# Optimization experiments

Measured on AMD Instinct MI355X. Metric: run time of the kernel, lower is better.

The kernel has to match this reference:

```python
import jax, jax.numpy as jnp
import numpy as np

B, J, DIMS, T = 1024, 22, 3, 100
C = J * DIMS            # 66 channels
H, HD = 8, 64           # heads, head_dim
E = H * HD              # 512
LOCAL_WINDOW = 5
EPS = 1e-5


def setup_inputs() -> dict:
    key = jax.random.key(0)
    ks = jax.random.split(key, 32)
    s = 0.02  # small init scale for learned params

    # kinematic-chain skeleton adjacency mask (buffer, symmetric 0/1)
    am = np.zeros((J, J), dtype=np.float32)
    for i in range(J - 1):
        am[i, i + 1] = 1.0
        am[i + 1, i] = 1.0
    adj_mask = jnp.asarray(am)

    # banded temporal mask: tril(+w) * triu(-w)
    tm = np.tril(np.ones((T, T), np.float32), LOCAL_WINDOW) * np.triu(np.ones((T, T), np.float32), -LOCAL_WINDOW)
    traj_mask = jnp.asarray(tm)

    def lin(k, din, dout):
        k1, k2 = jax.random.split(k)
        return (jax.random.normal(k1, (din, dout), jnp.float32) * s,
                jax.random.normal(k2, (dout,), jnp.float32) * s)

    # spatial->temporal attention: query_dim=C (66), key_dim=T (100)
    st_wq, st_bq = lin(ks[1], C, E)
    st_wk, st_bk = lin(ks[2], T, E)
    st_wv, st_bv = lin(ks[3], T, E)
    st_wo, st_bo = lin(ks[4], E, C)
    # temporal->spatial attention: query_dim=T (100), key_dim=C (66)
    ts_wq, ts_bq = lin(ks[5], T, E)
    ts_wk, ts_bk = lin(ks[6], C, E)
    ts_wv, ts_bv = lin(ks[7], C, E)
    ts_wo, ts_bo = lin(ks[8], E, T)

    return {
        "x": jax.random.normal(ks[0], (B, C, T), jnp.float32),
        "adj_mask": adj_mask,
        "s_adj": jnp.eye(J, dtype=jnp.float32),  # torch init: eye
        "traj_mask": traj_mask,
        # torch init is zeros; use small random so the temporal branch is non-degenerate
        "t_adj": jax.random.normal(ks[9], (T, T), jnp.float32) * s,
        "st_wq": st_wq, "st_bq": st_bq, "st_wk": st_wk, "st_bk": st_bk,
        "st_wv": st_wv, "st_bv": st_bv, "st_wo": st_wo, "st_bo": st_bo,
        "ts_wq": ts_wq, "ts_bq": ts_bq, "ts_wk": ts_wk, "ts_bk": ts_bk,
        "ts_wv": ts_wv, "ts_bv": ts_bv, "ts_wo": ts_wo, "ts_bo": ts_bo,
        "ln_alpha": jnp.ones((1, C, 1), jnp.float32),
        "ln_beta": jnp.zeros((1, C, 1), jnp.float32),
        "fc_w": jax.random.normal(ks[10], (T, T), jnp.float32) * s,  # torch Linear weight [out,in]
        "fc_b": jax.random.normal(ks[11], (T,), jnp.float32) * s,
    }


def _cross_attn(q, kv, wq, bq, wk, bk, wv, bv, wo, bo):
    # q: [B, Lq, qdim], kv: [B, Lk, kdim] -> [B, Lq, qdim]
    b = q.shape[0]
    Q = (q @ wq + bq).reshape(b, -1, H, HD)
    K = (kv @ wk + bk).reshape(b, -1, H, HD)
    V = (kv @ wv + bv).reshape(b, -1, H, HD)
    scores = jnp.einsum('bqhd,bkhd->bhqk', Q, K) / jnp.sqrt(jnp.float32(HD))
    attn = jax.nn.softmax(scores, axis=-1)
    out = jnp.einsum('bhqk,bkhd->bqhd', attn, V).reshape(b, -1, E)
    return out @ wo + bo


def reference(x, adj_mask, s_adj, traj_mask, t_adj,
              st_wq, st_bq, st_wk, st_bk, st_wv, st_bv, st_wo, st_bo,
              ts_wq, ts_bq, ts_wk, ts_bk, ts_wv, ts_bv, ts_wo, ts_bo,
              ln_alpha, ln_beta, fc_w, fc_b):
    b, c, t = x.shape
    j = c // DIMS

    # --- SpatialGC: symmetric degree-normalized masked adjacency conv ---
    deg = adj_mask.sum(axis=1)
    dis = jnp.where(deg > 0, deg ** -0.5, 0.0)
    A = s_adj * (adj_mask * dis[:, None] * dis[None, :])        # [J,J]
    spatial = jnp.einsum('vj,bjct->bvct', A, x.reshape(b, j, DIMS, t)).reshape(b, c, t)

    # --- TemporalGC: banded learned temporal adjacency ---
    temporal = jnp.einsum('ft,bnt->bnf', t_adj * traj_mask, x)   # [B,C,T]

    # --- CrossAttentiveGC ---
    sp_seq = spatial.transpose(0, 2, 1)                          # [B,T,C] spatial tokens
    tp_seq = temporal                                            # [B,C,T] temporal tokens
    enh_sp = _cross_attn(sp_seq, tp_seq, st_wq, st_bq, st_wk, st_bk, st_wv, st_bv, st_wo, st_bo)  # [B,T,C]
    enh_tp = _cross_attn(tp_seq, sp_seq, ts_wq, ts_bq, ts_wk, ts_bk, ts_wv, ts_bv, ts_wo, ts_bo)  # [B,C,T]
    combined = (enh_sp.reshape(b, t, j, DIMS).transpose(0, 2, 3, 1)
                + enh_tp.reshape(b, j, DIMS, t)).reshape(b, c, t)

    # --- LN over channel dim (dim=1) with biased variance ---
    mean = combined.mean(axis=1, keepdims=True)
    var = ((combined - mean) ** 2).mean(axis=1, keepdims=True)
    y = (combined - mean) / jnp.sqrt(var + EPS)
    y = y * ln_alpha + ln_beta

    # --- residual + Linear over the seq dim, tanh ---
    out = jnp.einsum('bct,ft->bcf', y + x, fc_w) + fc_b
    return jnp.tanh(out)
```

## Files before the change

### kernel.cpp

```cpp
#include <hip/hip_runtime.h>
#include <hip/hip_bf16.h>
#include <math.h>
#include <stdint.h>

typedef __hip_bfloat16 bf16;
typedef __attribute__((ext_vector_type(8))) short short8;
typedef __attribute__((ext_vector_type(4))) short short4v;
typedef __attribute__((ext_vector_type(4))) float f32x4;
typedef __attribute__((ext_vector_type(4))) unsigned int uint4v;
union PF { uint4v u; short8 s; };

#define CC 66
#define TT 100
#define JJ 22
#define HH 8
#define HD 64
#define EE 512
#define CPAD 101

#define SPT_R 112
#define SPT_S 96
#define TP_R 80
#define TP_S 128

#define W_STWK 0
#define W_STWQ 65536
#define W_TSWK 114688
#define W_TSWQ 163840
#define W_VST  229376
#define W_VTS  311296
#define W_TOTAL 397312

#define TOKSP 0
#define TOKTP 11648
#define G0Z1  22528
#define G0Z2  27648
#define G0Z3  34816
#define G1Z1  45056
#define G1Z2  52224
#define G1Z3  57344
#define SMEM_SH 71680

__device__ __forceinline__ bf16 f2b(float v){ return __float2bfloat16(v); }
__device__ __forceinline__ short sb(float v){ __hip_bfloat16 h = __float2bfloat16(v); return *(short*)&h; }
__device__ __forceinline__ unsigned int pk2(float a, float b){
  unsigned short ua = (unsigned short)sb(a), ub = (unsigned short)sb(b);
  return (unsigned int)ua | ((unsigned int)ub << 16);
}

__device__ __forceinline__ void tr_body(
    const float* __restrict__ src, bf16* __restrict__ dst,
    int Rsrc, int Csrc, int JP, int IP, int blk, int tid)
{
  int o = blk*256 + tid;
  if (o >= JP*IP) return;
  int j = o / IP, i = o - j*IP;
  float v = (j < Csrc && i < Rsrc) ? src[(long)i*Csrc + j] : 0.f;
  dst[o] = f2b(v);
}

__device__ __forceinline__ void wt_body(
    const float* __restrict__ wv, const float* __restrict__ wo,
    bf16* __restrict__ dst, int OUT, int KDIM, int OP, int KP, int blk, int tid)
{
  int idx = blk*256 + tid;
  if (idx >= 8*OP*KP) return;
  int o = idx % OP;
  int hk = idx / OP;
  int k = hk % KP, h = hk / KP;
  float acc = 0.f;
  if (o < OUT && k < KDIM) {
    const float* wvp = wv + (long)k*EE + h*64;
    const float* wop = wo + (long)(h*64)*OUT + o;
    #pragma unroll 8
    for (int d = 0; d < 64; ++d) acc += wvp[d] * wop[(long)d*OUT];
  }
  dst[(long)h*OP*KP + (long)o*KP + k] = f2b(acc);
}

__global__ __launch_bounds__(256) void k_wprep(
    const float* __restrict__ st_wk, const float* __restrict__ st_wq,
    const float* __restrict__ ts_wk, const float* __restrict__ ts_wq,
    const float* __restrict__ st_wv, const float* __restrict__ st_wo,
    const float* __restrict__ ts_wv, const float* __restrict__ ts_wo,
    const float* __restrict__ st_bo, const float* __restrict__ st_bv,
    const float* __restrict__ ts_bo, const float* __restrict__ ts_bv,
    bf16* __restrict__ wsec, float* __restrict__ bias2)
{
  const int blk = blockIdx.x, tid = threadIdx.x;
  if      (blk <  256) tr_body(st_wk, wsec + W_STWK, TT, EE, EE, 128, blk,      tid);
  else if (blk <  448) tr_body(st_wq, wsec + W_STWQ, CC, EE, EE,  96, blk-256,  tid);
  else if (blk <  640) tr_body(ts_wk, wsec + W_TSWK, CC, EE, EE,  96, blk-448,  tid);
  else if (blk <  896) tr_body(ts_wq, wsec + W_TSWQ, TT, EE, EE, 128, blk-640,  tid);
  else if (blk < 1216) wt_body(st_wv, st_wo, wsec + W_VST, CC, TT,  80, 128, blk-896,  tid);
  else if (blk < 1552) wt_body(ts_wv, ts_wo, wsec + W_VTS, TT, CC, 112,  96, blk-1216, tid);
  else {
    if (tid < 128) {
      int c = tid; float a = 0.f;
      if (c < CC) {
        a = st_bo[c];
        for (int e = 0; e < EE; ++e) a += st_bv[e] * st_wo[(long)e*CC + c];
      }
      bias2[tid] = a;
    } else {
      int t = tid - 128; float a = 0.f;
      if (t < TT) {
        a = ts_bo[t];
        for (int e = 0; e < EE; ++e) a += ts_bv[e] * ts_wo[(long)e*TT + t];
      }
      bias2[tid] = a;
    }
  }
}

__global__ __launch_bounds__(256) void k_prep(
    const float* __restrict__ x, const float* __restrict__ adj,
    const float* __restrict__ sadj, const float* __restrict__ tmask,
    const float* __restrict__ tadj,
    bf16* __restrict__ spT_all, bf16* __restrict__ tp_all)
{
  __shared__ float s_x[CC*TT];
  __shared__ float s_Mt[TT*TT];
  __shared__ float s_A[JJ*JJ];
  __shared__ float s_dis[JJ];
  const int b = blockIdx.x, tid = threadIdx.x;
  const long bb = (long)b * (CC*TT);

  if (tid < JJ) {
    float dsum = 0.f;
    for (int i = 0; i < JJ; ++i) dsum += adj[tid*JJ + i];
    s_dis[tid] = dsum > 0.f ? rsqrtf(dsum) : 0.f;
  }
  for (int o = tid; o < CC*TT; o += 256) s_x[o] = x[bb + o];
  for (int o = tid; o < TT*TT; o += 256) {
    int f = o / TT, t = o - f*TT;
    s_Mt[t*TT + f] = tadj[o] * tmask[o];
  }
  __syncthreads();
  for (int o = tid; o < JJ*JJ; o += 256) {
    int v = o / JJ, j = o - v*JJ;
    s_A[o] = sadj[o] * adj[o] * s_dis[v] * s_dis[j];
  }
  __syncthreads();

  bf16* spT = spT_all + (long)b * (SPT_R*SPT_S);
  bf16* tp  = tp_all  + (long)b * (TP_R*TP_S);

  for (int o = tid; o < 28*SPT_S; o += 256) {
    int t4 = o / SPT_S, c = o - t4*SPT_S;
    int t = t4*4;
    float ax=0.f, ay=0.f, az=0.f, aw=0.f;
    if (t < TT && c < CC) {
      int v = c/3, dd = c - v*3;
      for (int j = 0; j < JJ; ++j) {
        float av = s_A[v*JJ + j];
        float4 xv = *(const float4*)(s_x + (j*3+dd)*TT + t);
        ax += av*xv.x; ay += av*xv.y; az += av*xv.z; aw += av*xv.w;
      }
    }
    spT[(t  )*SPT_S + c] = f2b(ax);
    spT[(t+1)*SPT_S + c] = f2b(ay);
    spT[(t+2)*SPT_S + c] = f2b(az);
    spT[(t+3)*SPT_S + c] = f2b(aw);
  }
  for (int o = tid; o < TP_R*32; o += 256) {
    int n = o >> 5, f4 = o & 31;
    int f = f4*4;
    float ax=0.f, ay=0.f, az=0.f, aw=0.f;
    if (n < CC && f < TT) {
      for (int t = 0; t < TT; ++t) {
        float xv = s_x[n*TT + t];
        float4 w = *(const float4*)(s_Mt + t*TT + f);
        ax += xv*w.x; ay += xv*w.y; az += xv*w.z; aw += xv*w.w;
      }
    }
    short4v pk;
    pk.x = sb(ax); pk.y = sb(ay); pk.z = sb(az); pk.w = sb(aw);
    *(short4v*)(tp + n*TP_S + f) = pk;
  }
}

template<int Nt, int KCH, int SA, int SB>
__device__ __forceinline__ void build_kq(
    const short* __restrict__ W, const short* __restrict__ Tok,
    short* __restrict__ Z, const float* __restrict__ rowbias,
    int gw, int ln, int qd)
{
  const int mi = gw & 3;
  const int d0 = mi*16 + qd*4;
  const short* ap = W + (long)(mi*16 + ln)*SA;
  short8 af[KCH];
  #pragma unroll
  for (int kc = 0; kc < KCH; ++kc) af[kc] = *(const short8*)(ap + qd*8 + kc*32);
  float rb0=0.f, rb1=0.f, rb2=0.f, rb3=0.f;
  if (rowbias) { rb0=rowbias[d0]; rb1=rowbias[d0+1]; rb2=rowbias[d0+2]; rb3=rowbias[d0+3]; }
  constexpr int NU = (Nt + 1) / 2;
  #pragma unroll
  for (int u = 0; u < NU; ++u) {
    const int ni = (gw >> 2) + 2*u;
    if (ni < Nt) {
      const int row = ni*16 + ln;
      const short* bp = Tok + (long)row*SB;
      f32x4 acc = {0.f,0.f,0.f,0.f};
      #pragma unroll
      for (int kc = 0; kc < KCH; ++kc)
        acc = __builtin_amdgcn_mfma_f32_16x16x32_bf16(
            af[kc], *(const short8*)(bp + qd*8 + kc*32), acc, 0,0,0);
      short4v pk;
      pk.x = sb(acc[0]+rb0); pk.y = sb(acc[1]+rb1);
      pk.z = sb(acc[2]+rb2); pk.w = sb(acc[3]+rb3);
      *(short4v*)(Z + row*64 + (d0 ^ ((ln & 7) << 3))) = pk;
    }
  }
}

template<int Mt, int Nt, int KCH, int SA, int SB, int SZ>
__device__ __forceinline__ void build_vt(
    const short* __restrict__ Tok, const short* __restrict__ Wv,
    short* __restrict__ Z, int gw, int ln, int qd)
{
  if (gw >= Mt) return;
  const int mi = gw;
  const int k0 = mi*16 + qd*4;
  const short* ap = Tok + (long)(mi*16 + ln)*SA;
  short8 af[KCH];
  #pragma unroll
  for (int kc = 0; kc < KCH; ++kc) af[kc] = *(const short8*)(ap + qd*8 + kc*32);
  #pragma unroll
  for (int ni = 0; ni < Nt; ++ni) {
    const int row = ni*16 + ln;
    const short* bp = Wv + (long)row*SB;
    f32x4 acc = {0.f,0.f,0.f,0.f};
    #pragma unroll
    for (int kc = 0; kc < KCH; ++kc)
      acc = __builtin_amdgcn_mfma_f32_16x16x32_bf16(
          af[kc], *(const short8*)(bp + qd*8 + kc*32), acc, 0,0,0);
    short4v pk;
    pk.x = sb(acc[0]); pk.y = sb(acc[1]); pk.z = sb(acc[2]); pk.w = sb(acc[3]);
    *(short4v*)(Z + row*SZ + (k0 ^ ((ln & 7) << 3))) = pk;
  }
}

template<int A>
__device__ __forceinline__ void build_head(
    short* __restrict__ SMEM, const short* __restrict__ wsec,
    const float* __restrict__ bq, int h, int gw, int ln, int qd)
{
  constexpr int MQ  = A ? 5 : 7;
  constexpr int MKV = A ? 7 : 5;
  constexpr int MO  = A ? 7 : 5;
  constexpr int QCH = A ? 4 : 3;
  constexpr int KCH = A ? 3 : 4;
  constexpr int SWQ = A ? 128 : 96;
  constexpr int SWK = A ? 96 : 128;
  constexpr int SWV = A ? 96 : 128;
  constexpr int STQ = A ? 136 : 104;
  constexpr int STK = A ? 104 : 136;
  const short* tokq = SMEM + (A ? TOKTP : TOKSP);
  const short* tokk = SMEM + (A ? TOKSP : TOKTP);
  short* Z1 = SMEM + (A ? G1Z1 : G0Z1);
  short* Z2 = SMEM + (A ? G1Z2 : G0Z2);
  short* Z3 = SMEM + (A ? G1Z3 : G0Z3);
  const short* wkT = wsec + (A ? W_TSWK : W_STWK);
  const short* wqT = wsec + (A ? W_TSWQ : W_STWQ);
  const short* wvt = wsec + (A ? W_VTS  : W_VST);
  const int base = h * HD;
  build_kq<MKV, KCH, SWK, STK>(wkT + (long)base*SWK, tokk, Z1, nullptr, gw, ln, qd);
  build_kq<MQ,  QCH, SWQ, STQ>(wqT + (long)base*SWQ, tokq, Z2, bq + base, gw, ln, qd);
  build_vt<MKV, MO, KCH, STK, SWV, 128>(tokk, wvt + (long)h*(MO*16*SWV), Z3, gw, ln, qd);
}

template<int A>
__device__ __forceinline__ void chain_head(
    const short* __restrict__ SMEM, f32x4* __restrict__ accO,
    int gw, int ln, int qd)
{
  constexpr int KVR = A ? 100 : 66;
  constexpr int MQ  = A ? 5 : 7;
  constexpr int MKV = A ? 7 : 5;
  constexpr int MO  = A ? 7 : 5;
  constexpr int PCH = A ? 4 : 3;
  if (gw >= MQ) return;
  const short* Z1 = SMEM + (A ? G1Z1 : G0Z1);
  const short* Z2 = SMEM + (A ? G1Z2 : G0Z2);
  const short* Z3 = SMEM + (A ? G1Z3 : G0Z3);
  const int msk = (ln & 7) << 3;

  const short* bqp = Z2 + (gw*16 + ln)*64;
  const short8 qf0 = *(const short8*)(bqp + ((qd*8     ) ^ msk));
  const short8 qf1 = *(const short8*)(bqp + ((qd*8 + 32) ^ msk));
  f32x4 s[MKV];
  #pragma unroll
  for (int ni = 0; ni < MKV; ++ni) {
    const short* ap = Z1 + (ni*16 + ln)*64;
    f32x4 acc = {0.f,0.f,0.f,0.f};
    acc = __builtin_amdgcn_mfma_f32_16x16x32_bf16(
        *(const short8*)(ap + ((qd*8     ) ^ msk)), qf0, acc, 0,0,0);
    acc = __builtin_amdgcn_mfma_f32_16x16x32_bf16(
        *(const short8*)(ap + ((qd*8 + 32) ^ msk)), qf1, acc, 0,0,0);
    s[ni] = acc;
  }
  #pragma unroll
  for (int ni = 0; ni < MKV; ++ni) {
    #pragma unroll
    for (int r = 0; r < 4; ++r) {
      const int kv = ni*16 + qd*4 + r;
      s[ni][r] = (kv < KVR) ? s[ni][r]*0.125f : -1e30f;
    }
  }
  float mx = -1e30f;
  #pragma unroll
  for (int ni = 0; ni < MKV; ++ni)
    #pragma unroll
    for (int r = 0; r < 4; ++r) mx = fmaxf(mx, s[ni][r]);
  mx = fmaxf(mx, __shfl_xor(mx, 16));
  mx = fmaxf(mx, __shfl_xor(mx, 32));
  float l = 0.f;
  #pragma unroll
  for (int ni = 0; ni < MKV; ++ni)
    #pragma unroll
    for (int r = 0; r < 4; ++r) {
      float p = __expf(s[ni][r] - mx);
      s[ni][r] = p; l += p;
    }
  l += __shfl_xor(l, 16);
  l += __shfl_xor(l, 32);
  const float rs = 1.f / l;
  unsigned int plo[2*PCH], phi[2*PCH];
  #pragma unroll
  for (int ni = 0; ni < 2*PCH; ++ni) {
    if (ni < MKV) {
      plo[ni] = pk2(s[ni][0]*rs, s[ni][1]*rs);
      phi[ni] = pk2(s[ni][2]*rs, s[ni][3]*rs);
    } else { plo[ni] = 0u; phi[ni] = 0u; }
  }
  #pragma unroll
  for (int kc = 0; kc < PCH; ++kc) {
    PF pf;
    #pragma unroll
    for (int w = 0; w < 4; ++w) {
      const int srcLane = ln + 16*((qd & 1)*2 + (w >> 1));
      int va, vb;
      if (w & 1) {
        va = __shfl((int)phi[2*kc  ], srcLane, 64);
        vb = __shfl((int)phi[2*kc+1], srcLane, 64);
      } else {
        va = __shfl((int)plo[2*kc  ], srcLane, 64);
        vb = __shfl((int)plo[2*kc+1], srcLane, 64);
      }
      pf.u[w] = (qd < 2) ? (unsigned int)va : (unsigned int)vb;
    }
    #pragma unroll
    for (int oi = 0; oi < MO; ++oi) {
      const short* ap = Z3 + (oi*16 + ln)*128;
      short8 af = *(const short8*)(ap + ((qd*8 + kc*32) ^ msk));
      accO[oi] = __builtin_amdgcn_mfma_f32_16x16x32_bf16(af, pf.s, accO[oi], 0,0,0);
    }
  }
}

__global__ __launch_bounds__(1024, 1) void k_attn2(
    const bf16* __restrict__ spT_all, const bf16* __restrict__ tp_all,
    const bf16* __restrict__ wsec_,
    const float* __restrict__ st_bq, const float* __restrict__ ts_bq,
    const float* __restrict__ bias2, const float* __restrict__ x,
    const float* __restrict__ alpha, const float* __restrict__ beta,
    const float* __restrict__ fcw, const float* __restrict__ fcb,
    float* __restrict__ out)
{
  __shared__ __align__(16) short SMEM[SMEM_SH];
  const int b = blockIdx.x, tid = threadIdx.x;
  const long bb = (long)b * (CC*TT);
  const int wave = tid >> 6, lane = tid & 63, ln = lane & 15, qd = lane >> 4;
  const int g = wave >> 3, gw = wave & 7;
  const short* wsec = (const short*)wsec_;

  {
    const short* gsp = (const short*)(spT_all + (long)b*SPT_R*SPT_S);
    const short* gtp = (const short*)(tp_all  + (long)b*TP_R*TP_S);
    for (int o = tid; o < 112*12; o += 1024) {
      int r = o / 12, c8 = o - r*12;
      *(short8*)(SMEM + TOKSP + r*104 + c8*8) = *(const short8*)(gsp + r*SPT_S + c8*8);
    }
    for (int o = tid; o < 80*16; o += 1024) {
      int r = o >> 4, c8 = o & 15;
      *(short8*)(SMEM + TOKTP + r*136 + c8*8) = *(const short8*)(gtp + r*TP_S + c8*8);
    }
  }
  for (int o = tid; o < 80*16; o += 1024) {
    int r = o >> 4, kv = 80 + (o & 15);
    SMEM[G0Z3 + r*128 + (kv ^ ((r & 7) << 3))] = 0;
  }
  for (int o = tid; o < 112*16; o += 1024) {
    int r = o >> 4, kv = 112 + (o & 15);
    SMEM[G1Z3 + r*128 + (kv ^ ((r & 7) << 3))] = 0;
  }

  f32x4 accO[7];
  { f32x4 z = {0.f,0.f,0.f,0.f};
    #pragma unroll
    for (int i = 0; i < 7; ++i) accO[i] = z; }

  for (int h = 0; h < HH; ++h) {
    __syncthreads();
    if (g == 0) build_head<0>(SMEM, wsec, st_bq, h, gw, ln, qd);
    else        build_head<1>(SMEM, wsec, ts_bq, h, gw, ln, qd);
    __syncthreads();
    if (g == 0) chain_head<0>(SMEM, accO, gw, ln, qd);
    else        chain_head<1>(SMEM, accO, gw, ln, qd);
  }

  float* comb = (float*)(SMEM + G0Z1);
  float* s_w  = comb + 6668;
  __syncthreads();
  if (g == 0) {
    if (gw < 7) {
      const int t = gw*16 + ln;
      if (t < TT) {
        #pragma unroll
        for (int oi = 0; oi < 5; ++oi)
          #pragma unroll
          for (int r = 0; r < 4; ++r) {
            const int c = oi*16 + qd*4 + r;
            if (c < CC) comb[c*CPAD + t] = accO[oi][r];
          }
      }
    }
  } else {
    for (int o = tid - 512; o < TT*TT; o += 512) {
      int f = o / TT, t = o - f*TT;
      s_w[t*TT + f] = fcw[o];
    }
  }
  __syncthreads();
  if (g == 1 && gw < 5) {
    const int c = gw*16 + ln;
    if (c < CC) {
      #pragma unroll
      for (int oi = 0; oi < 7; ++oi)
        #pragma unroll
        for (int r = 0; r < 4; ++r) {
          const int t = oi*16 + qd*4 + r;
          if (t < TT) comb[c*CPAD + t] += accO[oi][r];
        }
    }
  }
  __syncthreads();
  for (int o = tid; o < CC*TT; o += 1024) {
    int c = o / TT, t = o - c*TT;
    comb[c*CPAD + t] += bias2[c] + bias2[128 + t];
  }
  __syncthreads();
  if (tid < 2*TT) {
    const int t = tid >> 1, hf = tid & 1;
    float part = 0.f;
    for (int c = hf; c < CC; c += 2) part += comb[c*CPAD + t];
    float mean = (part + __shfl_xor(part, 1)) * (1.f/CC);
    float vp = 0.f;
    for (int c = hf; c < CC; c += 2) { float dv = comb[c*CPAD + t] - mean; vp += dv*dv; }
    float var = (vp + __shfl_xor(vp, 1)) * (1.f/CC);
    float rstd = 1.f / sqrtf(var + 1e-5f);
    for (int c = hf; c < CC; c += 2) {
      float y = (comb[c*CPAD + t] - mean) * rstd * alpha[c] + beta[c];
      comb[c*CPAD + t] = y + x[bb + c*TT + t];
    }
  }
  __syncthreads();
  for (int o = tid; o < CC*25; o += 1024) {
    int c = o / 25, f4 = o - c*25;
    int f = f4*4;
    const float* cr = comb + c*CPAD;
    float ax=0.f, ay=0.f, az=0.f, aw=0.f;
    for (int t = 0; t < TT; ++t) {
      float xv = cr[t];
      float4 w = *(const float4*)(s_w + t*TT + f);
      ax += xv*w.x; ay += xv*w.y; az += xv*w.z; aw += xv*w.w;
    }
    float4 r4;
    r4.x = tanhf(ax + fcb[f  ]); r4.y = tanhf(ay + fcb[f+1]);
    r4.z = tanhf(az + fcb[f+2]); r4.w = tanhf(aw + fcb[f+3]);
    *(float4*)(out + bb + c*TT + f) = r4;
  }
}

__global__ __launch_bounds__(128) void k_fused(
    const float* __restrict__ x, const float* __restrict__ adj,
    const float* __restrict__ sadj, const float* __restrict__ tmask,
    const float* __restrict__ tadj,
    const float* __restrict__ st_wq, const float* __restrict__ st_bq,
    const float* __restrict__ st_wk, const float* __restrict__ st_bk,
    const float* __restrict__ st_wv, const float* __restrict__ st_bv,
    const float* __restrict__ st_wo, const float* __restrict__ st_bo,
    const float* __restrict__ ts_wq, const float* __restrict__ ts_bq,
    const float* __restrict__ ts_wk, const float* __restrict__ ts_bk,
    const float* __restrict__ ts_wv, const float* __restrict__ ts_bv,
    const float* __restrict__ ts_wo, const float* __restrict__ ts_bo,
    const float* __restrict__ alpha, const float* __restrict__ beta,
    const float* __restrict__ fcw, const float* __restrict__ fcb,
    float* __restrict__ out)
{
  __shared__ float s_sp[CC*TT];
  __shared__ float s_tp[CC*TT];
  __shared__ __align__(16) float s_kv[2*TT*HD];
  __shared__ float s_comb[CC*CPAD];
  __shared__ float s_A[JJ*JJ];
  __shared__ float s_dis[JJ];

  const int b = blockIdx.x, tid = threadIdx.x;
  const long bb = (long)b * (CC*TT);
  float* s_xs = s_comb;
  float* s_Mt = s_kv;

  if (tid < JJ) {
    float dsum = 0.f;
    for (int i = 0; i < JJ; ++i) dsum += adj[tid*JJ + i];
    s_dis[tid] = dsum > 0.f ? rsqrtf(dsum) : 0.f;
  }
  for (int o = tid; o < CC*TT; o += 128) s_xs[o] = x[bb + o];
  for (int o = tid; o < TT*TT; o += 128) {
    int f = o / TT, t = o - f*TT;
    s_Mt[t*TT + f] = tadj[o] * tmask[o];
  }
  __syncthreads();
  for (int o = tid; o < JJ*JJ; o += 128) {
    int v = o / JJ, j = o - v*JJ;
    s_A[o] = sadj[o] * adj[o] * s_dis[v] * s_dis[j];
  }
  __syncthreads();

  for (int o = tid; o < CC*TT; o += 128) {
    int c = o / TT, t = o - c*TT, v = c / 3, dd = c - v*3;
    float acc = 0.f;
    for (int j = 0; j < JJ; ++j) acc += s_A[v*JJ + j] * s_xs[(j*3 + dd)*TT + t];
    s_sp[o] = acc;
  }
  for (int o = tid; o < CC*TT; o += 128) {
    int n = o / TT, f = o - n*TT;
    float a0 = 0.f, a1 = 0.f;
    for (int t = 0; t < TT; t += 2) {
      a0 += s_xs[n*TT + t    ] * s_Mt[(t    )*TT + f];
      a1 += s_xs[n*TT + t + 1] * s_Mt[(t + 1)*TT + f];
    }
    s_tp[o] = a0 + a1;
  }
  __syncthreads();

  for (int o = tid; o < CC*TT; o += 128) {
    int c = o / TT, t = o - c*TT;
    s_comb[c*CPAD + t] = st_bo[c] + ts_bo[t];
  }

  {
    float* s_k = s_kv;
    float* s_v = s_kv + TT*HD;
    for (int h = 0; h < HH; ++h) {
      const int base = h*HD;
      __syncthreads();
      {
        const int d = tid & 63, krow = tid >> 6;
// ... 122 lines not shown
          for (int i = 0; i < 16; ++i) {
            float4 vv4 = vr4[i];
            ov[4*i  ] = ov[4*i  ]*corr + p*vv4.x;
            ov[4*i+1] = ov[4*i+1]*corr + p*vv4.y;
            ov[4*i+2] = ov[4*i+2]*corr + p*vv4.z;
            ov[4*i+3] = ov[4*i+3]*corr + p*vv4.w;
          }
          m = mn;
        }
        float rl = 1.f/l;
        #pragma unroll
        for (int d = 0; d < HD; ++d) ov[d] *= rl;
        for (int t = 0; t < TT; ++t) {
          const float* wr = ts_wo + (long)base*TT + t;
          float a0=0.f,a1=0.f,a2=0.f,a3=0.f;
          #pragma unroll
          for (int d = 0; d < HD; d += 4) {
            a0 += ov[d  ]*wr[(long)(d  )*TT]; a1 += ov[d+1]*wr[(long)(d+1)*TT];
            a2 += ov[d+2]*wr[(long)(d+2)*TT]; a3 += ov[d+3]*wr[(long)(d+3)*TT];
          }
          s_comb[q*CPAD + t] += a0+a1+a2+a3;
        }
      }
    }
  }
  __syncthreads();

  if (tid < TT) {
    const int t = tid;
    float mean = 0.f;
    for (int c = 0; c < CC; ++c) mean += s_comb[c*CPAD + t];
    mean *= (1.f/CC);
    float var = 0.f;
    for (int c = 0; c < CC; ++c) { float dv = s_comb[c*CPAD + t] - mean; var += dv*dv; }
    var *= (1.f/CC);
    float rstd = 1.f / sqrtf(var + 1e-5f);
    for (int c = 0; c < CC; ++c) {
      float y = (s_comb[c*CPAD + t] - mean) * rstd * alpha[c] + beta[c];
      s_comb[c*CPAD + t] = y + x[bb + c*TT + t];
    }
  }
  __syncthreads();

  float* s_w = s_kv;
  for (int o = tid; o < TT*TT; o += 128) {
    int f = o / TT, t = o - f*TT;
    s_w[t*TT + f] = fcw[o];
  }
  __syncthreads();

  for (int o = tid; o < CC*TT; o += 128) {
    int c = o / TT, f = o - c*TT;
    const float* cr = s_comb + c*CPAD;
    float a0 = 0.f, a1 = 0.f;
    for (int t = 0; t < TT; t += 2) {
      a0 += cr[t    ] * s_w[(t    )*TT + f];
      a1 += cr[t + 1] * s_w[(t + 1)*TT + f];
    }
    out[bb + o] = tanhf(a0 + a1 + fcb[f]);
  }
}

extern "C" void kernel_launch(void* const* d_in, const int* in_sizes, int n_in,
                              void* d_out, int out_size, void* d_ws, size_t ws_size,
                              hipStream_t stream) {
  const float* x     = (const float*)d_in[0];
  const float* adj   = (const float*)d_in[1];
  const float* sadj  = (const float*)d_in[2];
  const float* tmask = (const float*)d_in[3];
  const float* tadj  = (const float*)d_in[4];
  const float* st_wq = (const float*)d_in[5];  const float* st_bq = (const float*)d_in[6];
  const float* st_wk = (const float*)d_in[7];  const float* st_bk = (const float*)d_in[8];
  const float* st_wv = (const float*)d_in[9];  const float* st_bv = (const float*)d_in[10];
  const float* st_wo = (const float*)d_in[11]; const float* st_bo = (const float*)d_in[12];
  const float* ts_wq = (const float*)d_in[13]; const float* ts_bq = (const float*)d_in[14];
  const float* ts_wk = (const float*)d_in[15]; const float* ts_bk = (const float*)d_in[16];
  const float* ts_wv = (const float*)d_in[17]; const float* ts_bv = (const float*)d_in[18];
  const float* ts_wo = (const float*)d_in[19]; const float* ts_bo = (const float*)d_in[20];
  const float* alpha = (const float*)d_in[21]; const float* beta  = (const float*)d_in[22];
  const float* fcw   = (const float*)d_in[23]; const float* fcb   = (const float*)d_in[24];
  float* out = (float*)d_out;

  const int B = in_sizes[0] / (CC*TT);
  const size_t w_bytes   = (size_t)W_TOTAL * 2 + 1024;
  const size_t spt_bytes = (size_t)B * SPT_R * SPT_S * 2;
  const size_t tp_bytes  = (size_t)B * TP_R * TP_S * 2;
  const size_t need = w_bytes + spt_bytes + tp_bytes;

  if (ws_size >= need) {
    bf16*  wsec    = (bf16*)d_ws;
    float* bias2   = (float*)((char*)d_ws + (size_t)W_TOTAL*2);
    bf16*  spT_all = (bf16*)((char*)d_ws + w_bytes);
    bf16*  tp_all  = spT_all + (size_t)B * SPT_R * SPT_S;

    k_wprep<<<1553, 256, 0, stream>>>(st_wk, st_wq, ts_wk, ts_wq,
                                      st_wv, st_wo, ts_wv, ts_wo,
                                      st_bo, st_bv, ts_bo, ts_bv,
                                      wsec, bias2);
    k_prep<<<B, 256, 0, stream>>>(x, adj, sadj, tmask, tadj, spT_all, tp_all);
    k_attn2<<<B, 1024, 0, stream>>>(spT_all, tp_all, wsec, st_bq, ts_bq,
                                    bias2, x, alpha, beta, fcw, fcb, out);
  } else {
    k_fused<<<B, 128, 0, stream>>>(x, adj, sadj, tmask, tadj,
                                   st_wq, st_bq, st_wk, st_bk, st_wv, st_bv, st_wo, st_bo,
                                   ts_wq, ts_bq, ts_wk, ts_bk, ts_wv, ts_bv, ts_wo, ts_bo,
                                   alpha, beta, fcw, fcb, out);
  }
}
```

Measured before the change: 674.9 us.

## Run both attention directions sequentially across all 16 waves with shared-memory P matrix

Stops splitting the 16 waves into two groups that each handle one attention direction at once. Now all waves process one direction at a time, across all heads. The softmax probabilities are written to a shared-memory P buffer instead of being shuffled across lanes. The P·V output is computed as independent tiles spread over all waves and accumulated straight into the shared comb buffer, rather than kept in per-wave register accumulators. This cuts register pressure and balances work across waves, at the cost of an extra barrier per head and read-modify-write traffic on the shared comb buffer.

Measured after the change: 786.9 us. 1.17x slower.

```diff
diff --git a/kernel.cpp b/kernel.cpp
--- a/kernel.cpp
+++ b/kernel.cpp
@@ -7,8 +7,6 @@
 typedef __attribute__((ext_vector_type(8))) short short8;
 typedef __attribute__((ext_vector_type(4))) short short4v;
 typedef __attribute__((ext_vector_type(4))) float f32x4;
-typedef __attribute__((ext_vector_type(4))) unsigned int uint4v;
-union PF { uint4v u; short8 s; };
 
 #define CC 66
 #define TT 100
@@ -33,20 +31,13 @@
 
 #define TOKSP 0
 #define TOKTP 11648
-#define G0Z1  22528
-#define G0Z2  27648
-#define G0Z3  34816
-#define G1Z1  45056
-#define G1Z2  52224
-#define G1Z3  57344
-#define SMEM_SH 71680
+#define ZONES 22528
+#define PBUF  49152
+#define COMBO 64384
+#define SMEM_SH 77728
 
 __device__ __forceinline__ bf16 f2b(float v){ return __float2bfloat16(v); }
 __device__ __forceinline__ short sb(float v){ __hip_bfloat16 h = __float2bfloat16(v); return *(short*)&h; }
-__device__ __forceinline__ unsigned int pk2(float a, float b){
-  unsigned short ua = (unsigned short)sb(a), ub = (unsigned short)sb(b);
-  return (unsigned int)ua | ((unsigned int)ub << 16);
-}
 
 __device__ __forceinline__ void tr_body(
     const float* __restrict__ src, bf16* __restrict__ dst,
@@ -181,12 +172,12 @@
 }
 
 template<int Nt, int KCH, int SA, int SB>
-__device__ __forceinline__ void build_kq(
+__device__ __forceinline__ void build_kq16(
     const short* __restrict__ W, const short* __restrict__ Tok,
     short* __restrict__ Z, const float* __restrict__ rowbias,
-    int gw, int ln, int qd)
-{
-  const int mi = gw & 3;
+    int w, int ln, int qd)
+{
+  const int mi = w & 3;
   const int d0 = mi*16 + qd*4;
   const short* ap = W + (long)(mi*16 + ln)*SA;
   short8 af[KCH];
@@ -194,10 +185,10 @@
   for (int kc = 0; kc < KCH; ++kc) af[kc] = *(const short8*)(ap + qd*8 + kc*32);
   float rb0=0.f, rb1=0.f, rb2=0.f, rb3=0.f;
   if (rowbias) { rb0=rowbias[d0]; rb1=rowbias[d0+1]; rb2=rowbias[d0+2]; rb3=rowbias[d0+3]; }
-  constexpr int NU = (Nt + 1) / 2;
+  constexpr int NU = (Nt + 3) / 4;
   #pragma unroll
   for (int u = 0; u < NU; ++u) {
-    const int ni = (gw >> 2) + 2*u;
+    const int ni = (w >> 2) + 4*u;
     if (ni < Nt) {
       const int row = ni*16 + ln;
       const short* bp = Tok + (long)row*SB;
@@ -214,152 +205,166 @@
   }
 }
 
-template<int Mt, int Nt, int KCH, int SA, int SB, int SZ>
-__device__ __forceinline__ void build_vt(
+template<int Mt, int Nt, int KCH, int SA, int SB>
+__device__ __forceinline__ void build_vt16(
     const short* __restrict__ Tok, const short* __restrict__ Wv,
-    short* __restrict__ Z, int gw, int ln, int qd)
-{
-  if (gw >= Mt) return;
-  const int mi = gw;
+    short* __restrict__ Z, int w, int ln, int qd)
+{
+  const int mi = w >> 1;
+  if (mi >= Mt) return;
   const int k0 = mi*16 + qd*4;
   const short* ap = Tok + (long)(mi*16 + ln)*SA;
   short8 af[KCH];
   #pragma unroll
   for (int kc = 0; kc < KCH; ++kc) af[kc] = *(const short8*)(ap + qd*8 + kc*32);
+  constexpr int NU = (Nt + 1) / 2;
   #pragma unroll
-  for (int ni = 0; ni < Nt; ++ni) {
-    const int row = ni*16 + ln;
-    const short* bp = Wv + (long)row*SB;
-    f32x4 acc = {0.f,0.f,0.f,0.f};
-    #pragma unroll
-    for (int kc = 0; kc < KCH; ++kc)
-      acc = __builtin_amdgcn_mfma_f32_16x16x32_bf16(
-          af[kc], *(const short8*)(bp + qd*8 + kc*32), acc, 0,0,0);
-    short4v pk;
-    pk.x = sb(acc[0]); pk.y = sb(acc[1]); pk.z = sb(acc[2]); pk.w = sb(acc[3]);
-    *(short4v*)(Z + row*SZ + (k0 ^ ((ln & 7) << 3))) = pk;
+  for (int u = 0; u < NU; ++u) {
+    const int ni = (w & 1) + 2*u;
+    if (ni < Nt) {
+      const int row = ni*16 + ln;
+      const short* bp = Wv + (long)row*SB;
+      f32x4 acc = {0.f,0.f,0.f,0.f};
+      #pragma unroll
+      for (int kc = 0; kc < KCH; ++kc)
+        acc = __builtin_amdgcn_mfma_f32_16x16x32_bf16(
+            af[kc], *(const short8*)(bp + qd*8 + kc*32), acc, 0,0,0);
+      short4v pk;
+      pk.x = sb(acc[0]); pk.y = sb(acc[1]); pk.z = sb(acc[2]); pk.w = sb(acc[3]);
+      *(short4v*)(Z + row*128 + (k0 ^ ((ln & 7) << 3))) = pk;
+    }
   }
 }
 
 template<int A>
-__device__ __forceinline__ void build_head(
+__device__ __forceinline__ void flavor_pass(
     short* __restrict__ SMEM, const short* __restrict__ wsec,
-    const float* __restrict__ bq, int h, int gw, int ln, int qd)
-{
+    const float* __restrict__ bq_all,
+    int tid, int w, int ln, int qd)
+{
+  constexpr int QROWS = A ? 66 : 100;
+  constexpr int KVR   = A ? 100 : 66;
+  constexpr int OUTD  = A ? 100 : 66;
   constexpr int MQ  = A ? 5 : 7;
   constexpr int MKV = A ? 7 : 5;
   constexpr int MO  = A ? 7 : 5;
   constexpr int QCH = A ? 4 : 3;
   constexpr int KCH = A ? 3 : 4;
+  constexpr int PCH = A ? 4 : 3;
   constexpr int SWQ = A ? 128 : 96;
   constexpr int SWK = A ? 96 : 128;
   constexpr int SWV = A ? 96 : 128;
   constexpr int STQ = A ? 136 : 104;
   constexpr int STK = A ? 104 : 136;
+
   const short* tokq = SMEM + (A ? TOKTP : TOKSP);
   const short* tokk = SMEM + (A ? TOKSP : TOKTP);
-  short* Z1 = SMEM + (A ? G1Z1 : G0Z1);
-  short* Z2 = SMEM + (A ? G1Z2 : G0Z2);
-  short* Z3 = SMEM + (A ? G1Z3 : G0Z3);
+  short* Z1 = SMEM + ZONES;
+  short* Z2 = Z1 + MKV*16*64;
+  short* Z3 = Z2 + MQ*16*64;
+  short* Pm = SMEM + PBUF;
+  float* comb = (float*)(SMEM + COMBO);
   const short* wkT = wsec + (A ? W_TSWK : W_STWK);
   const short* wqT = wsec + (A ? W_TSWQ : W_STWQ);
   const short* wvt = wsec + (A ? W_VTS  : W_VST);
-  const int base = h * HD;
-  build_kq<MKV, KCH, SWK, STK>(wkT + (long)base*SWK, tokk, Z1, nullptr, gw, ln, qd);
-  build_kq<MQ,  QCH, SWQ, STQ>(wqT + (long)base*SWQ, tokq, Z2, bq + base, gw, ln, qd);
-  build_vt<MKV, MO, KCH, STK, SWV, 128>(tokk, wvt + (long)h*(MO*16*SWV), Z3, gw, ln, qd);
-}
-
-template<int A>
-__device__ __forceinline__ void chain_head(
-    const short* __restrict__ SMEM, f32x4* __restrict__ accO,
-    int gw, int ln, int qd)
-{
-  constexpr int KVR = A ? 100 : 66;
-  constexpr int MQ  = A ? 5 : 7;
-  constexpr int MKV = A ? 7 : 5;
-  constexpr int MO  = A ? 7 : 5;
-  constexpr int PCH = A ? 4 : 3;
-  if (gw >= MQ) return;
-  const short* Z1 = SMEM + (A ? G1Z1 : G0Z1);
-  const short* Z2 = SMEM + (A ? G1Z2 : G0Z2);
-  const short* Z3 = SMEM + (A ? G1Z3 : G0Z3);
-  const int msk = (ln & 7) << 3;
-
-  const short* bqp = Z2 + (gw*16 + ln)*64;
-  const short8 qf0 = *(const short8*)(bqp + ((qd*8     ) ^ msk));
-  const short8 qf1 = *(const short8*)(bqp + ((qd*8 + 32) ^ msk));
-  f32x4 s[MKV];
-  #pragma unroll
-  for (int ni = 0; ni < MKV; ++ni) {
-    const short* ap = Z1 + (ni*16 + ln)*64;
-    f32x4 acc = {0.f,0.f,0.f,0.f};
-    acc = __builtin_amdgcn_mfma_f32_16x16x32_bf16(
-        *(const short8*)(ap + ((qd*8     ) ^ msk)), qf0, acc, 0,0,0);
-    acc = __builtin_amdgcn_mfma_f32_16x16x32_bf16(
-        *(const short8*)(ap + ((qd*8 + 32) ^ msk)), qf1, acc, 0,0,0);
-    s[ni] = acc;
-  }
-  #pragma unroll
-  for (int ni = 0; ni < MKV; ++ni) {
-    #pragma unroll
-    for (int r = 0; r < 4; ++r) {
-      const int kv = ni*16 + qd*4 + r;
-      s[ni][r] = (kv < KVR) ? s[ni][r]*0.125f : -1e30f;
-    }
-  }
-  float mx = -1e30f;
-  #pragma unroll
-  for (int ni = 0; ni < MKV; ++ni)
-    #pragma unroll
-    for (int r = 0; r < 4; ++r) mx = fmaxf(mx, s[ni][r]);
-  mx = fmaxf(mx, __shfl_xor(mx, 16));
-  mx = fmaxf(mx, __shfl_xor(mx, 32));
-  float l = 0.f;
-  #pragma unroll
-  for (int ni = 0; ni < MKV; ++ni)
-    #pragma unroll
-    for (int r = 0; r < 4; ++r) {
-      float p = __expf(s[ni][r] - mx);
-      s[ni][r] = p; l += p;
-    }
-  l += __shfl_xor(l, 16);
-  l += __shfl_xor(l, 32);
-  const float rs = 1.f / l;
-  unsigned int plo[2*PCH], phi[2*PCH];
-  #pragma unroll
-  for (int ni = 0; ni < 2*PCH; ++ni) {
-    if (ni < MKV) {
-      plo[ni] = pk2(s[ni][0]*rs, s[ni][1]*rs);
-      phi[ni] = pk2(s[ni][2]*rs, s[ni][3]*rs);
-    } else { plo[ni] = 0u; phi[ni] = 0u; }
-  }
-  #pragma unroll
-  for (int kc = 0; kc < PCH; ++kc) {
-    PF pf;
-    #pragma unroll
-    for (int w = 0; w < 4; ++w) {
-      const int srcLane = ln + 16*((qd & 1)*2 + (w >> 1));
-      int va, vb;
-      if (w & 1) {
-        va = __shfl((int)phi[2*kc  ], srcLane, 64);
-        vb = __shfl((int)phi[2*kc+1], srcLane, 64);
-      } else {
-        va = __shfl((int)plo[2*kc  ], srcLane, 64);
-        vb = __shfl((int)plo[2*kc+1], srcLane, 64);
-      }
-      pf.u[w] = (qd < 2) ? (unsigned int)va : (unsigned int)vb;
-    }
-    #pragma unroll
-    for (int oi = 0; oi < MO; ++oi) {
+
+  for (int o = tid; o < MO*16*16; o += 1024) {
+    const int r = o >> 4, kv = MKV*16 + (o & 15);
+    Z3[r*128 + (kv ^ ((r & 7) << 3))] = 0;
+  }
+
+  for (int h = 0; h < HH; ++h) {
+    const int base = h*HD;
+    __syncthreads();
+    build_kq16<MKV, KCH, SWK, STK>(wkT + (long)base*SWK, tokk, Z1, nullptr, w, ln, qd);
+    build_kq16<MQ,  QCH, SWQ, STQ>(wqT + (long)base*SWQ, tokq, Z2, bq_all + base, w, ln, qd);
+    build_vt16<MKV, MO, KCH, STK, SWV>(tokk, wvt + (long)h*(MO*16*SWV), Z3, w, ln, qd);
+    __syncthreads();
+
+    if (w < MQ) {
+      const int msk = (ln & 7) << 3;
+      const short* bqp = Z2 + (w*16 + ln)*64;
+      const short8 qf0 = *(const short8*)(bqp + ((qd*8     ) ^ msk));
+      const short8 qf1 = *(const short8*)(bqp + ((qd*8 + 32) ^ msk));
+      f32x4 s[MKV];
+      #pragma unroll
+      for (int ni = 0; ni < MKV; ++ni) {
+        const short* ap = Z1 + (ni*16 + ln)*64;
+        f32x4 acc = {0.f,0.f,0.f,0.f};
+        acc = __builtin_amdgcn_mfma_f32_16x16x32_bf16(
+            *(const short8*)(ap + ((qd*8     ) ^ msk)), qf0, acc, 0,0,0);
+        acc = __builtin_amdgcn_mfma_f32_16x16x32_bf16(
+            *(const short8*)(ap + ((qd*8 + 32) ^ msk)), qf1, acc, 0,0,0);
+        s[ni] = acc;
+      }
+      #pragma unroll
+      for (int ni = 0; ni < MKV; ++ni) {
+        #pragma unroll
+        for (int r = 0; r < 4; ++r) {
+          const int kv = ni*16 + qd*4 + r;
+          s[ni][r] = (kv < KVR) ? s[ni][r]*0.125f : -1e30f;
+        }
+      }
+      float mx = -1e30f;
+      #pragma unroll
+      for (int ni = 0; ni < MKV; ++ni)
+        #pragma unroll
+        for (int r = 0; r < 4; ++r) mx = fmaxf(mx, s[ni][r]);
+      mx = fmaxf(mx, __shfl_xor(mx, 16));
+      mx = fmaxf(mx, __shfl_xor(mx, 32));
+      float l = 0.f;
+      #pragma unroll
+      for (int ni = 0; ni < MKV; ++ni)
+        #pragma unroll
+        for (int r = 0; r < 4; ++r) {
+          float p = __expf(s[ni][r] - mx);
+          s[ni][r] = p; l += p;
+        }
+      l += __shfl_xor(l, 16);
+      l += __shfl_xor(l, 32);
+      const float rs = 1.f / l;
+      short* pr = Pm + (w*16 + ln)*136;
+      #pragma unroll
+      for (int ni = 0; ni < 2*PCH; ++ni) {
+        short4v pk;
+        if (ni < MKV) {
+          pk.x = sb(s[ni][0]*rs); pk.y = sb(s[ni][1]*rs);
+          pk.z = sb(s[ni][2]*rs); pk.w = sb(s[ni][3]*rs);
+        } else {
+          pk.x = 0; pk.y = 0; pk.z = 0; pk.w = 0;
+        }
+        *(short4v*)(pr + ni*16 + qd*4) = pk;
+      }
+    }
+    __syncthreads();
+
+    for (int ti = w; ti < MQ*MO; ti += 16) {
+      const int qi = ti / MO, oi = ti - qi*MO;
+      const int msk = (ln & 7) << 3;
       const short* ap = Z3 + (oi*16 + ln)*128;
-      short8 af = *(const short8*)(ap + ((qd*8 + kc*32) ^ msk));
-      accO[oi] = __builtin_amdgcn_mfma_f32_16x16x32_bf16(af, pf.s, accO[oi], 0,0,0);
-    }
-  }
-}
-
-__global__ __launch_bounds__(1024, 1) void k_attn2(
+      const short* bp = Pm + (qi*16 + ln)*136;
+      f32x4 acc = {0.f,0.f,0.f,0.f};
+      #pragma unroll
+      for (int kc = 0; kc < PCH; ++kc)
+        acc = __builtin_amdgcn_mfma_f32_16x16x32_bf16(
+            *(const short8*)(ap + ((qd*8 + kc*32) ^ msk)),
+            *(const short8*)(bp + qd*8 + kc*32), acc, 0,0,0);
+      const int q = qi*16 + ln;
+      if (q < QROWS) {
+        #pragma unroll
+        for (int r = 0; r < 4; ++r) {
+          const int outc = oi*16 + qd*4 + r;
+          if (outc < OUTD) {
+            const int idx = A ? (q*CPAD + outc) : (outc*CPAD + q);
+            comb[idx] += acc[r];
+          }
+        }
+      }
+    }
+  }
+}
+
+__global__ __launch_bounds__(1024) void k_attn2(
     const bf16* __restrict__ spT_all, const bf16* __restrict__ tp_all,
     const bf16* __restrict__ wsec_,
     const float* __restrict__ st_bq, const float* __restrict__ ts_bq,
@@ -371,9 +376,9 @@
   __shared__ __align__(16) short SMEM[SMEM_SH];
   const int b = blockIdx.x, tid = threadIdx.x;
   const long bb = (long)b * (CC*TT);
-  const int wave = tid >> 6, lane = tid & 63, ln = lane & 15, qd = lane >> 4;
-  const int g = wave >> 3, gw = wave & 7;
+  const int w = tid >> 6, lane = tid & 63, ln = lane & 15, qd = lane >> 4;
   const short* wsec = (const short*)wsec_;
+  float* comb = (float*)(SMEM + COMBO);
 
   {
     const short* gsp = (const short*)(spT_all + (long)b*SPT_R*SPT_S);
@@ -386,66 +391,19 @@
       int r = o >> 4, c8 = o & 15;
       *(short8*)(SMEM + TOKTP + r*136 + c8*8) = *(const short8*)(gtp + r*TP_S + c8*8);
     }
-  }
-  for (int o = tid; o < 80*16; o += 1024) {
-    int r = o >> 4, kv = 80 + (o & 15);
-    SMEM[G0Z3 + r*128 + (kv ^ ((r & 7) << 3))] = 0;
-  }
-  for (int o = tid; o < 112*16; o += 1024) {
-    int r = o >> 4, kv = 112 + (o & 15);
-    SMEM[G1Z3 + r*128 + (kv ^ ((r & 7) << 3))] = 0;
-  }
-
-  f32x4 accO[7];
-  { f32x4 z = {0.f,0.f,0.f,0.f};
-    #pragma unroll
-    for (int i = 0; i < 7; ++i) accO[i] = z; }
-
-  for (int h = 0; h < HH; ++h) {
-    __syncthreads();
-    if (g == 0) build_head<0>(SMEM, wsec, st_bq, h, gw, ln, qd);
-    else        build_head<1>(SMEM, wsec, ts_bq, h, gw, ln, qd);
-    __syncthreads();
-    if (g == 0) chain_head<0>(SMEM, accO, gw, ln, qd);
-    else        chain_head<1>(SMEM, accO, gw, ln, qd);
-  }
-
-  float* comb = (float*)(SMEM + G0Z1);
-  float* s_w  = comb + 6668;
-  __syncthreads();
-  if (g == 0) {
-    if (gw < 7) {
-      const int t = gw*16 + ln;
-      if (t < TT) {
-        #pragma unroll
-        for (int oi = 0; oi < 5; ++oi)
-          #pragma unroll
-          for (int r = 0; r < 4; ++r) {
-            const int c = oi*16 + qd*4 + r;
-            if (c < CC) comb[c*CPAD + t] = accO[oi][r];
-          }
-      }
-    }
-  } else {
-    for (int o = tid - 512; o < TT*TT; o += 512) {
-      int f = o / TT, t = o - f*TT;
-      s_w[t*TT + f] = fcw[o];
-    }
-  }
-  __syncthreads();
-  if (g == 1 && gw < 5) {
-    const int c = gw*16 + ln;
-    if (c < CC) {
-      #pragma unroll
-      for (int oi = 0; oi < 7; ++oi)
-        #pragma unroll
-        for (int r = 0; r < 4; ++r) {
-          const int t = oi*16 + qd*4 + r;
-          if (t < TT) comb[c*CPAD + t] += accO[oi][r];
-        }
-    }
-  }
-  __syncthreads();
+    for (int o = tid; o < CC*CPAD; o += 1024) comb[o] = 0.f;
+  }
+
+  flavor_pass<0>(SMEM, wsec, st_bq, tid, w, ln, qd);
+  __syncthreads();
+  flavor_pass<1>(SMEM, wsec, ts_bq, tid, w, ln, qd);
+
+  float* s_w = (float*)(SMEM + ZONES);
+  __syncthreads();
+  for (int o = tid; o < TT*TT; o += 1024) {
+    int f = o / TT, t = o - f*TT;
+    s_w[t*TT + f] = fcw[o];
+  }
   for (int o = tid; o < CC*TT; o += 1024) {
     int c = o / TT, t = o - c*TT;
     comb[c*CPAD + t] += bias2[c] + bias2[128 + t];
@@ -473,8 +431,8 @@
     float ax=0.f, ay=0.f, az=0.f, aw=0.f;
     for (int t = 0; t < TT; ++t) {
       float xv = cr[t];
-      float4 w = *(const float4*)(s_w + t*TT + f);
-      ax += xv*w.x; ay += xv*w.y; az += xv*w.z; aw += xv*w.w;
+      float4 wv = *(const float4*)(s_w + t*TT + f);
+      ax += xv*wv.x; ay += xv*wv.y; az += xv*wv.z; aw += xv*wv.w;
     }
     float4 r4;
     r4.x = tanhf(ax + fcb[f  ]); r4.y = tanhf(ay + fcb[f+1]);
```

## Fuse spatial/temporal token prep into attention kernel via shared memory

Applied to the files above, without the earlier changes.

Removes the separate k_prep kernel and computes the spatial and temporal GCN token tiles directly inside k_attn2. The inputs x, the masked temporal adjacency and the normalized spatial adjacency are staged in the kernel's shared-memory region and written straight to the LDS token layout. This avoids a kernel launch and the global-memory round trip of bf16 token buffers. In exchange the 1024-thread attention block does the small prep GEMMs itself, with extra barriers before attention starts. The second launch-bounds argument is also dropped.

Result: no change. 682.1 us (+1.1%).

```diff
diff --git a/kernel.cpp b/kernel.cpp
--- a/kernel.cpp
+++ b/kernel.cpp
@@ -17,11 +17,6 @@
 #define HD 64
 #define EE 512
 #define CPAD 101
-
-#define SPT_R 112
-#define SPT_S 96
-#define TP_R 80
-#define TP_S 128
 
 #define W_STWK 0
 #define W_STWQ 65536
@@ -40,6 +35,10 @@
 #define G1Z2  52224
 #define G1Z3  57344
 #define SMEM_SH 71680
+#define P_SX  22528
+#define P_SMT 35728
+#define P_SA  55728
+#define P_SDIS 56696
 
 __device__ __forceinline__ bf16 f2b(float v){ return __float2bfloat16(v); }
 __device__ __forceinline__ short sb(float v){ __hip_bfloat16 h = __float2bfloat16(v); return *(short*)&h; }
@@ -110,73 +109,6 @@
       }
       bias2[tid] = a;
     }
-  }
-}
-
-__global__ __launch_bounds__(256) void k_prep(
-    const float* __restrict__ x, const float* __restrict__ adj,
-    const float* __restrict__ sadj, const float* __restrict__ tmask,
-    const float* __restrict__ tadj,
-    bf16* __restrict__ spT_all, bf16* __restrict__ tp_all)
-{
-  __shared__ float s_x[CC*TT];
-  __shared__ float s_Mt[TT*TT];
-  __shared__ float s_A[JJ*JJ];
-  __shared__ float s_dis[JJ];
-  const int b = blockIdx.x, tid = threadIdx.x;
-  const long bb = (long)b * (CC*TT);
-
-  if (tid < JJ) {
-    float dsum = 0.f;
-    for (int i = 0; i < JJ; ++i) dsum += adj[tid*JJ + i];
-    s_dis[tid] = dsum > 0.f ? rsqrtf(dsum) : 0.f;
-  }
-  for (int o = tid; o < CC*TT; o += 256) s_x[o] = x[bb + o];
-  for (int o = tid; o < TT*TT; o += 256) {
-    int f = o / TT, t = o - f*TT;
-    s_Mt[t*TT + f] = tadj[o] * tmask[o];
-  }
-  __syncthreads();
-  for (int o = tid; o < JJ*JJ; o += 256) {
-    int v = o / JJ, j = o - v*JJ;
-    s_A[o] = sadj[o] * adj[o] * s_dis[v] * s_dis[j];
-  }
-  __syncthreads();
-
-  bf16* spT = spT_all + (long)b * (SPT_R*SPT_S);
-  bf16* tp  = tp_all  + (long)b * (TP_R*TP_S);
-
-  for (int o = tid; o < 28*SPT_S; o += 256) {
-    int t4 = o / SPT_S, c = o - t4*SPT_S;
-    int t = t4*4;
-    float ax=0.f, ay=0.f, az=0.f, aw=0.f;
-    if (t < TT && c < CC) {
-      int v = c/3, dd = c - v*3;
-      for (int j = 0; j < JJ; ++j) {
-        float av = s_A[v*JJ + j];
-        float4 xv = *(const float4*)(s_x + (j*3+dd)*TT + t);
-        ax += av*xv.x; ay += av*xv.y; az += av*xv.z; aw += av*xv.w;
-      }
-    }
-    spT[(t  )*SPT_S + c] = f2b(ax);
-    spT[(t+1)*SPT_S + c] = f2b(ay);
-    spT[(t+2)*SPT_S + c] = f2b(az);
-    spT[(t+3)*SPT_S + c] = f2b(aw);
-  }
-  for (int o = tid; o < TP_R*32; o += 256) {
-    int n = o >> 5, f4 = o & 31;
-    int f = f4*4;
-    float ax=0.f, ay=0.f, az=0.f, aw=0.f;
-    if (n < CC && f < TT) {
-      for (int t = 0; t < TT; ++t) {
-        float xv = s_x[n*TT + t];
-        float4 w = *(const float4*)(s_Mt + t*TT + f);
-        ax += xv*w.x; ay += xv*w.y; az += xv*w.z; aw += xv*w.w;
-      }
-    }
-    short4v pk;
-    pk.x = sb(ax); pk.y = sb(ay); pk.z = sb(az); pk.w = sb(aw);
-    *(short4v*)(tp + n*TP_S + f) = pk;
   }
 }
 
@@ -359,11 +291,13 @@
   }
 }
 
-__global__ __launch_bounds__(1024, 1) void k_attn2(
-    const bf16* __restrict__ spT_all, const bf16* __restrict__ tp_all,
+__global__ __launch_bounds__(1024) void k_attn2(
+    const float* __restrict__ x, const float* __restrict__ adj,
+    const float* __restrict__ sadj, const float* __restrict__ tmask,
+    const float* __restrict__ tadj,
     const bf16* __restrict__ wsec_,
     const float* __restrict__ st_bq, const float* __restrict__ ts_bq,
-    const float* __restrict__ bias2, const float* __restrict__ x,
+    const float* __restrict__ bias2,
     const float* __restrict__ alpha, const float* __restrict__ beta,
     const float* __restrict__ fcw, const float* __restrict__ fcb,
     float* __restrict__ out)
@@ -375,18 +309,59 @@
   const int g = wave >> 3, gw = wave & 7;
   const short* wsec = (const short*)wsec_;
 
-  {
-    const short* gsp = (const short*)(spT_all + (long)b*SPT_R*SPT_S);
-    const short* gtp = (const short*)(tp_all  + (long)b*TP_R*TP_S);
-    for (int o = tid; o < 112*12; o += 1024) {
-      int r = o / 12, c8 = o - r*12;
-      *(short8*)(SMEM + TOKSP + r*104 + c8*8) = *(const short8*)(gsp + r*SPT_S + c8*8);
-    }
-    for (int o = tid; o < 80*16; o += 1024) {
-      int r = o >> 4, c8 = o & 15;
-      *(short8*)(SMEM + TOKTP + r*136 + c8*8) = *(const short8*)(gtp + r*TP_S + c8*8);
-    }
-  }
+  float* s_x  = (float*)(SMEM + P_SX);
+  float* s_Mt = (float*)(SMEM + P_SMT);
+  float* s_A  = (float*)(SMEM + P_SA);
+  float* s_dis= (float*)(SMEM + P_SDIS);
+  if (tid < JJ) {
+    float dsum = 0.f;
+    for (int i = 0; i < JJ; ++i) dsum += adj[tid*JJ + i];
+    s_dis[tid] = dsum > 0.f ? rsqrtf(dsum) : 0.f;
+  }
+  for (int o = tid; o < CC*TT; o += 1024) s_x[o] = x[bb + o];
+  for (int o = tid; o < TT*TT; o += 1024) {
+    int f = o / TT, t = o - f*TT;
+    s_Mt[t*TT + f] = tadj[o] * tmask[o];
+  }
+  __syncthreads();
+  for (int o = tid; o < JJ*JJ; o += 1024) {
+    int v = o / JJ, j = o - v*JJ;
+    s_A[o] = sadj[o] * adj[o] * s_dis[v] * s_dis[j];
+  }
+  __syncthreads();
+  for (int o = tid; o < 28*104; o += 1024) {
+    int t4 = o / 104, c = o - t4*104;
+    int t = t4*4;
+    float ax=0.f, ay=0.f, az=0.f, aw=0.f;
+    if (t < TT && c < CC) {
+      int v = c/3, dd = c - v*3;
+      for (int j = 0; j < JJ; ++j) {
+        float av = s_A[v*JJ + j];
+        float4 xv = *(const float4*)(s_x + (j*3+dd)*TT + t);
+        ax += av*xv.x; ay += av*xv.y; az += av*xv.z; aw += av*xv.w;
+      }
+    }
+    SMEM[TOKSP + (t  )*104 + c] = sb(ax);
+    SMEM[TOKSP + (t+1)*104 + c] = sb(ay);
+    SMEM[TOKSP + (t+2)*104 + c] = sb(az);
+    SMEM[TOKSP + (t+3)*104 + c] = sb(aw);
+  }
+  for (int o = tid; o < 80*34; o += 1024) {
+    int n = o / 34, f4 = o - n*34;
+    int f = f4*4;
+    float ax=0.f, ay=0.f, az=0.f, aw=0.f;
+    if (n < CC && f < TT) {
+      for (int t = 0; t < TT; ++t) {
+        float xv = s_x[n*TT + t];
+        float4 w = *(const float4*)(s_Mt + t*TT + f);
+        ax += xv*w.x; ay += xv*w.y; az += xv*w.z; aw += xv*w.w;
+      }
+    }
+    short4v pk;
+    pk.x = sb(ax); pk.y = sb(ay); pk.z = sb(az); pk.w = sb(aw);
+    *(short4v*)(SMEM + TOKTP + n*136 + f) = pk;
+  }
+  __syncthreads();
   for (int o = tid; o < 80*16; o += 1024) {
     int r = o >> 4, kv = 80 + (o & 15);
     SMEM[G0Z3 + r*128 + (kv ^ ((r & 7) << 3))] = 0;
@@ -473,8 +448,8 @@
     float ax=0.f, ay=0.f, az=0.f, aw=0.f;
     for (int t = 0; t < TT; ++t) {
       float xv = cr[t];
-      float4 w = *(const float4*)(s_w + t*TT + f);
-      ax += xv*w.x; ay += xv*w.y; az += xv*w.z; aw += xv*w.w;
+      float4 wv = *(const float4*)(s_w + t*TT + f);
+      ax += xv*wv.x; ay += xv*wv.y; az += xv*wv.z; aw += xv*wv.w;
     }
     float4 r4;
     r4.x = tanhf(ax + fcb[f  ]); r4.y = tanhf(ay + fcb[f+1]);
@@ -763,24 +738,19 @@
   float* out = (float*)d_out;
 
   const int B = in_sizes[0] / (CC*TT);
-  const size_t w_bytes   = (size_t)W_TOTAL * 2 + 1024;
-  const size_t spt_bytes = (size_t)B * SPT_R * SPT_S * 2;
-  const size_t tp_bytes  = (size_t)B * TP_R * TP_S * 2;
-  const size_t need = w_bytes + spt_bytes + tp_bytes;
+  const size_t need = (size_t)W_TOTAL * 2 + 1024;
 
   if (ws_size >= need) {
-    bf16*  wsec    = (bf16*)d_ws;
-    float* bias2   = (float*)((char*)d_ws + (size_t)W_TOTAL*2);
-    bf16*  spT_all = (bf16*)((char*)d_ws + w_bytes);
-    bf16*  tp_all  = spT_all + (size_t)B * SPT_R * SPT_S;
+    bf16*  wsec  = (bf16*)d_ws;
+    float* bias2 = (float*)((char*)d_ws + (size_t)W_TOTAL*2);
 
     k_wprep<<<1553, 256, 0, stream>>>(st_wk, st_wq, ts_wk, ts_wq,
                                       st_wv, st_wo, ts_wv, ts_wo,
                                       st_bo, st_bv, ts_bo, ts_bv,
                                       wsec, bias2);
-    k_prep<<<B, 256, 0, stream>>>(x, adj, sadj, tmask, tadj, spT_all, tp_all);
-    k_attn2<<<B, 1024, 0, stream>>>(spT_all, tp_all, wsec, st_bq, ts_bq,
-                                    bias2, x, alpha, beta, fcw, fcb, out);
+    k_attn2<<<B, 1024, 0, stream>>>(x, adj, sadj, tmask, tadj, wsec,
+                                    st_bq, ts_bq, bias2,
+                                    alpha, beta, fcw, fcb, out);
   } else {
     k_fused<<<B, 128, 0, stream>>>(x, adj, sadj, tmask, tadj,
                                    st_wq, st_bq, st_wk, st_bk, st_wv, st_bv, st_wo, st_bo,
```
